# Kernel optimization log

Measured on AMD Instinct MI355X. Metric: run time of the kernel, lower is better.

Reference implementation:

```python
import jax, jax.numpy as jnp
from jax import lax
import numpy as np

B, T, F, U = 256, 150, 1024, 28


def setup_inputs() -> dict:
    key = jax.random.key(0)
    ks = jax.random.split(key, 10)
    s = 0.05  # keep tanh/sigmoid unsaturated, ~glorot magnitude
    return {
        "x": jax.random.normal(ks[0], (B, T, F), jnp.float32),
        "Wa": jax.random.normal(ks[1], (U, F), jnp.float32) * s,
        "Ua": jax.random.normal(ks[2], (F, F), jnp.float32) * s,
        "Va": jax.random.normal(ks[3], (F, 1), jnp.float32) * s,
        "Ba1": jax.random.normal(ks[4], (1, F), jnp.float32) * s,
        "Ba2": jax.random.normal(ks[5], (1, F), jnp.float32) * s,
        "Ba3": jax.random.normal(ks[6], (1, 1), jnp.float32) * s,
        "gru_kernel": jax.random.normal(ks[7], (F, 3 * U), jnp.float32) * s,
        "gru_rkernel": jax.random.normal(ks[8], (U, 3 * U), jnp.float32) * s,
        "gru_bias": jax.random.normal(ks[9], (2, 3 * U), jnp.float32) * s,
    }


def reference(x, Wa, Ua, Va, Ba1, Ba2, Ba3, gru_kernel, gru_rkernel, gru_bias):
    b, t, f = x.shape
    u = Wa.shape[0]
    # UaH is loop-invariant in the original (x @ Ua + Ba2 each step) -> hoist it.
    UaH = jnp.einsum('btf,fg->btg', x, Ua) + Ba2  # (B,T,F)

    def step(h, _):
        # Bahdanau attention conditioned on previous GRU state h (B,U)
        WaS = h @ Wa + Ba1                                    # (B,F)
        scores = jnp.einsum('btf,fo->bt', jnp.tanh(UaH + WaS[:, None, :]), Va) + Ba3[0, 0]
        a = jax.nn.softmax(scores, axis=1)                    # (B,T)
        ctx = jnp.einsum('btf,bt->bf', x, a)                  # (B,F)
        # Keras GRUCell (reset_after=True)
        xz = ctx @ gru_kernel + gru_bias[0]                   # (B,3U)
        hz = h @ gru_rkernel + gru_bias[1]                    # (B,3U)
        x_z, x_r, x_h = jnp.split(xz, 3, axis=-1)
        r_z, r_r, r_h = jnp.split(hz, 3, axis=-1)
        z = jax.nn.sigmoid(x_z + r_z)
        r = jax.nn.sigmoid(x_r + r_r)
        hh = jnp.tanh(x_h + r * r_h)
        h_new = z * h + (1.0 - z) * hh
        return h_new, h_new

    h0 = jnp.zeros((b, u), x.dtype)
    _, ys = lax.scan(step, h0, None, length=t)  # (T,B,U)
    return jnp.transpose(ys, (1, 0, 2))         # (B,T,U)
```

## Files before the change

### kernel.cpp

```cpp
#include <hip/hip_runtime.h>
#include <hip/hip_bf16.h>


typedef _Float16 h8 __attribute__((ext_vector_type(8)));
typedef _Float16 h4 __attribute__((ext_vector_type(4)));
typedef _Float16 h2 __attribute__((ext_vector_type(2)));
typedef float    f4 __attribute__((ext_vector_type(4)));
typedef float    f2 __attribute__((ext_vector_type(2)));

#define B_   256
#define T_   150
#define F_   1024
#define U_   28
#define TU3  84

#define C2LOG2E 2.8853900817779268f
#define LOG2E   1.4426950408889634f

__device__ __forceinline__ float fast_exp(float x) {
    return __builtin_amdgcn_exp2f(x * LOG2E);
}
__device__ __forceinline__ float fast_sigmoid(float x) {
    float e = __builtin_amdgcn_exp2f(-x * LOG2E);
    return __builtin_amdgcn_rcpf(1.0f + e);
}
__device__ __forceinline__ float fast_tanh(float x) {
    float e = __builtin_amdgcn_exp2f(x * C2LOG2E);
    float r = __builtin_amdgcn_rcpf(e + 1.0f);
    return 1.0f - 2.0f * r;
}

__global__ void k_cvt(const float* __restrict__ in, _Float16* __restrict__ out, int n4) {
    int i = blockIdx.x * blockDim.x + threadIdx.x;
    int stride = gridDim.x * blockDim.x;
    const f4* in4 = (const f4*)in;
    h4* out4 = (h4*)out;
    for (; i < n4; i += stride) {
        f4 v = in4[i];
        h4 o;
        o[0] = (_Float16)v[0]; o[1] = (_Float16)v[1];
        o[2] = (_Float16)v[2]; o[3] = (_Float16)v[3];
        out4[i] = o;
    }
}

__global__ void k_cvt_transpose(const float* __restrict__ in, _Float16* __restrict__ out) {
    int idx = blockIdx.x * blockDim.x + threadIdx.x;
    int r = idx >> 10, c = idx & 1023;
    out[(c << 10) + r] = (_Float16)in[idx];
}

#define BM 128
#define BN 128
#define BK 32
#define LDT 40

__global__ __launch_bounds__(256) void k_gemm(
    const _Float16* __restrict__ A,
    const _Float16* __restrict__ Bt,
    const float*    __restrict__ bias,
    _Float16*       __restrict__ C)
{
    __shared__ _Float16 As[BM][LDT];
    __shared__ _Float16 Bs[BN][LDT];
    const int K = 1024;
    int bm = blockIdx.y, bn = blockIdx.x;
    int tid = threadIdx.x;
    int lane = tid & 63, wid = tid >> 6;
    int wm = wid >> 1, wn = wid & 1;
    f4 acc[4][4];
#pragma unroll
    for (int i = 0; i < 4; i++)
#pragma unroll
        for (int j = 0; j < 4; j++) { f4 z = {0.f, 0.f, 0.f, 0.f}; acc[i][j] = z; }

    int row0 = bm * BM, col0 = bn * BN;
    for (int kt = 0; kt < K; kt += BK) {
#pragma unroll
        for (int p = 0; p < 2; ++p) {
            int s = tid + p * 256;
            int r = s >> 2, seg = s & 3;
            h8 va = *(const h8*)(A  + (size_t)(row0 + r) * K + kt + seg * 8);
            *(h8*)(&As[r][seg * 8]) = va;
            h8 vb = *(const h8*)(Bt + (size_t)(col0 + r) * K + kt + seg * 8);
            *(h8*)(&Bs[r][seg * 8]) = vb;
        }
        __syncthreads();
        int kq = (lane >> 4) * 8;
        h8 af[4], bf[4];
#pragma unroll
        for (int mi = 0; mi < 4; mi++) af[mi] = *(const h8*)(&As[wm * 64 + mi * 16 + (lane & 15)][kq]);
#pragma unroll
        for (int ni = 0; ni < 4; ni++) bf[ni] = *(const h8*)(&Bs[wn * 64 + ni * 16 + (lane & 15)][kq]);
#pragma unroll
        for (int mi = 0; mi < 4; mi++)
#pragma unroll
            for (int ni = 0; ni < 4; ni++)
                acc[mi][ni] = __builtin_amdgcn_mfma_f32_16x16x32_f16(af[mi], bf[ni], acc[mi][ni], 0, 0, 0);
        __syncthreads();
    }
    int rq = (lane >> 4) * 4, cq = lane & 15;
#pragma unroll
    for (int mi = 0; mi < 4; mi++)
#pragma unroll
        for (int ni = 0; ni < 4; ni++) {
            int gc = col0 + wn * 64 + ni * 16 + cq;
            float bv = bias[gc];
#pragma unroll
            for (int j = 0; j < 4; j++) {
                int gr = row0 + wm * 64 + mi * 16 + rq + j;
                C[(size_t)gr * 1024 + gc] = (_Float16)(acc[mi][ni][j] + bv);
            }
        }
}

#define XLD 72

__global__ __launch_bounds__(256) void k_gemm_xg(
    const _Float16* __restrict__ A,
    const float*    __restrict__ gk,
    _Float16*       __restrict__ C)
{
    __shared__ _Float16 As[128][XLD];
    __shared__ _Float16 Bs[96][XLD];
    int tid = threadIdx.x;
    int lane = tid & 63, wid = tid >> 6;
    int wm = wid >> 1, wn = wid & 1;
    int row0 = blockIdx.x * 128;
    f4 acc[4][3];
#pragma unroll
    for (int i = 0; i < 4; i++)
#pragma unroll
        for (int j = 0; j < 3; j++) { f4 z = {0.f, 0.f, 0.f, 0.f}; acc[i][j] = z; }

    if (tid < 432) { h2 z; z[0] = (_Float16)0.f; z[1] = (_Float16)0.f; ((h2*)&Bs[84][0])[tid] = z; }

    for (int kt = 0; kt < 1024; kt += 64) {
#pragma unroll
        for (int p = 0; p < 4; ++p) {
            int s = tid + p * 256;
            int r = s >> 3, seg = s & 7;
            *(h8*)(&As[r][seg * 8]) = *(const h8*)(A + (size_t)(row0 + r) * 1024 + kt + seg * 8);
        }
#pragma unroll
        for (int p = 0; p < 21; ++p) {
            int s = tid + p * 256;
            int j = s % 84, k = s / 84;
            Bs[j][k] = (_Float16)gk[(size_t)(kt + k) * 84 + j];
        }
        __syncthreads();
#pragma unroll
        for (int kk = 0; kk < 64; kk += 32) {
            int kq = kk + (lane >> 4) * 8;
            h8 af[4], bf[3];
#pragma unroll
            for (int mi = 0; mi < 4; mi++) af[mi] = *(const h8*)(&As[wm * 64 + mi * 16 + (lane & 15)][kq]);
#pragma unroll
            for (int ni = 0; ni < 3; ni++) bf[ni] = *(const h8*)(&Bs[wn * 48 + ni * 16 + (lane & 15)][kq]);
#pragma unroll
            for (int mi = 0; mi < 4; mi++)
#pragma unroll
                for (int ni = 0; ni < 3; ni++)
                    acc[mi][ni] = __builtin_amdgcn_mfma_f32_16x16x32_f16(af[mi], bf[ni], acc[mi][ni], 0, 0, 0);
        }
        __syncthreads();
    }
    int rq = (lane >> 4) * 4, cq = lane & 15;
#pragma unroll
    for (int mi = 0; mi < 4; mi++)
#pragma unroll
        for (int ni = 0; ni < 3; ni++) {
            int gc = wn * 48 + ni * 16 + cq;
            if (gc < 84) {
#pragma unroll
                for (int j = 0; j < 4; j++) {
                    int gr = row0 + wm * 64 + mi * 16 + rq + j;
                    C[(size_t)gr * 84 + gc] = (_Float16)acc[mi][ni][j];
                }
            }
        }
}

__global__ __launch_bounds__(1024) void k_recur2(
    const _Float16* __restrict__ uah,
    const _Float16* __restrict__ xg,
    const float* __restrict__ Wa,
    const float* __restrict__ Va,
    const float* __restrict__ Ba1,
    const float* __restrict__ grk,
    const float* __restrict__ gbias,
    float* __restrict__ out)
{
    __shared__ _Float16 sWa[U_ * F_];
    __shared__ _Float16 sXG[T_ * TU3];
    __shared__ float sWaS[F_];
    __shared__ float sScore[160];
    __shared__ float sPart[8 * TU3];
    __shared__ float sGrk[U_ * TU3];
    __shared__ float sHz[TU3];
    __shared__ float sH[U_];
    __shared__ float sDen;

    int b = blockIdx.x;
    int tid = threadIdx.x;
    int lane = tid & 63, wvid = tid >> 6;

    for (int i = tid; i < U_ * F_; i += 1024) sWa[i] = (_Float16)Wa[i];
    {
        const _Float16* xgb = xg + (size_t)b * T_ * TU3;
        for (int i = tid; i < T_ * TU3; i += 1024) sXG[i] = xgb[i];
    }
    for (int i = tid; i < U_ * TU3; i += 1024) sGrk[i] = grk[i];
    if (tid < U_) sH[tid] = 0.f;

    float rBa1 = Ba1[tid];
    float rA0[8], rA1[8], vaBase = 0.f;
    {
        f4 a0 = *(const f4*)(Va + 8 * lane);
        f4 a1 = *(const f4*)(Va + 8 * lane + 4);
        f4 b0 = *(const f4*)(Va + 512 + 8 * lane);
        f4 b1 = *(const f4*)(Va + 512 + 8 * lane + 4);
#pragma unroll
        for (int e = 0; e < 4; ++e) {
            rA0[e] = -2.f * a0[e]; rA0[4 + e] = -2.f * a1[e];
            rA1[e] = -2.f * b0[e]; rA1[4 + e] = -2.f * b1[e];
            vaBase += a0[e] + a1[e] + b0[e] + b1[e];
        }
    }
    int p4c = tid / TU3, p4j = tid - p4c * TU3;
    bool p4on = tid < 8 * TU3;
    bool denon = (wvid == 13);
    bool hzon = (tid >= 896) && (tid < 896 + TU3);
    int hj = tid - 896;
    float rGb1 = hzon ? gbias[TU3 + hj] : 0.f;
    float rG0 = 0.f, rG1 = 0.f, rG2 = 0.f;
    if (tid < U_) { rG0 = gbias[tid]; rG1 = gbias[U_ + tid]; rG2 = gbias[2 * U_ + tid]; }
    __syncthreads();

    const _Float16* ub = uah + (size_t)b * T_ * F_;
    float* ob = out + (size_t)b * T_ * U_;

    for (int t = 0; t < T_; ++t) {
        {
            float acc = rBa1;
#pragma unroll
            for (int u = 0; u < U_; ++u) acc += sH[u] * (float)sWa[u * F_ + tid];
            sWaS[tid] = acc;
        }
        __syncthreads();
        float rW0[8], rW1[8];
        {
            f4 a0 = *(const f4*)(sWaS + 8 * lane);
            f4 a1 = *(const f4*)(sWaS + 8 * lane + 4);
            f4 b0 = *(const f4*)(sWaS + 512 + 8 * lane);
            f4 b1 = *(const f4*)(sWaS + 512 + 8 * lane + 4);
#pragma unroll
            for (int e = 0; e < 4; ++e) {
                rW0[e] = a0[e] * C2LOG2E; rW0[4 + e] = a1[e] * C2LOG2E;
                rW1[e] = b0[e] * C2LOG2E; rW1[4 + e] = b1[e] * C2LOG2E;
            }
        }
        {
            int r = wvid;
            const h8* pr = (const h8*)(ub + (size_t)r * F_);
            h8 u0 = pr[lane], u1 = pr[64 + lane];
            while (r < T_) {
                int rn = r + 16;
                h8 n0, n1;
                if (rn < T_) {
                    const h8* pn = (const h8*)(ub + (size_t)rn * F_);
                    n0 = pn[lane]; n1 = pn[64 + lane];
                }
                float acc = vaBase;
#pragma unroll
                for (int e = 0; e < 8; ++e) {
                    float t0 = fmaf((float)u0[e], C2LOG2E, rW0[e]);
                    float r0 = __builtin_amdgcn_rcpf(__builtin_amdgcn_exp2f(t0) + 1.0f);
                    acc = fmaf(rA0[e], r0, acc);
                    float t1 = fmaf((float)u1[e], C2LOG2E, rW1[e]);
                    float r1 = __builtin_amdgcn_rcpf(__builtin_amdgcn_exp2f(t1) + 1.0f);
                    acc = fmaf(rA1[e], r1, acc);
                }
#pragma unroll
                for (int off = 32; off; off >>= 1) acc += __shfl_xor(acc, off, 64);
                if (lane == 0) sScore[r] = fast_exp(acc);
                u0 = n0; u1 = n1; r = rn;
            }
        }
        __syncthreads();
        if (p4on) {
            float acc = 0.f;
            for (int r = p4c; r < T_; r += 8)
                acc = fmaf((float)sXG[r * TU3 + p4j], sScore[r], acc);
            sPart[p4c * TU3 + p4j] = acc;
        }
        if (denon) {
            float d0 = (lane < T_)       ? sScore[lane]       : 0.f;
            float d1 = (lane + 64 < T_)  ? sScore[lane + 64]  : 0.f;
            float d2 = (lane + 128 < T_) ? sScore[lane + 128] : 0.f;
            float ds = d0 + d1 + d2;
#pragma unroll
            for (int off = 32; off; off >>= 1) ds += __shfl_xor(ds, off, 64);
            if (lane == 0) sDen = ds;
        }
        if (hzon) {
            float hz = rGb1;
#pragma unroll
            for (int u = 0; u < U_; ++u) hz += sH[u] * sGrk[u * TU3 + hj];
            sHz[hj] = hz;
        }
        __syncthreads();
        if (tid < U_) {
            float rs = __builtin_amdgcn_rcpf(sDen);
            float x0 = 0.f, x1 = 0.f, x2 = 0.f;
#pragma unroll
            for (int c = 0; c < 8; ++c) {
                x0 += sPart[c * TU3 + tid];
                x1 += sPart[c * TU3 + U_ + tid];
                x2 += sPart[c * TU3 + 2 * U_ + tid];
            }
            x0 = fmaf(x0, rs, rG0);
            x1 = fmaf(x1, rs, rG1);
            x2 = fmaf(x2, rs, rG2);
            float z  = fast_sigmoid(x0 + sHz[tid]);
            float r  = fast_sigmoid(x1 + sHz[U_ + tid]);
            float hh = fast_tanh(x2 + r * sHz[2 * U_ + tid]);
            float hn = z * sH[tid] + (1.f - z) * hh;
            sH[tid] = hn;
            ob[(size_t)t * U_ + tid] = hn;
        }
        __syncthreads();
    }
}

extern "C" void kernel_launch(void* const* d_in, const int* in_sizes, int n_in,
                              void* d_out, int out_size, void* d_ws, size_t ws_size,
                              hipStream_t stream) {
    (void)in_sizes; (void)n_in; (void)out_size; (void)ws_size;
    const float* x   = (const float*)d_in[0];
    const float* Wa  = (const float*)d_in[1];
    const float* Ua  = (const float*)d_in[2];
    const float* Va  = (const float*)d_in[3];
    const float* Ba1 = (const float*)d_in[4];
    const float* Ba2 = (const float*)d_in[5];
    const float* gk  = (const float*)d_in[7];
    const float* grk = (const float*)d_in[8];
    const float* gb  = (const float*)d_in[9];
    float* out = (float*)d_out;

    const size_t NX = (size_t)B_ * T_ * F_;
    _Float16* xh  = (_Float16*)d_ws;
    _Float16* uat = xh + NX;
    _Float16* uah = uat + (size_t)F_ * F_;
    _Float16* xgh = uah + NX;

    k_cvt<<<2048, 256, 0, stream>>>(x, xh, (int)(NX / 4));
    k_cvt_transpose<<<(F_ * F_) / 256, 256, 0, stream>>>(Ua, uat);
    dim3 gg(F_ / BN, (B_ * T_) / BM);
    k_gemm<<<gg, 256, 0, stream>>>(xh, uat, Ba2, uah);
    k_gemm_xg<<<(B_ * T_) / 128, 256, 0, stream>>>(xh, gk, xgh);
    k_recur2<<<B_, 1024, 0, stream>>>(uah, xgh, Wa, Va, Ba1, grk, gb, out);
}
```

Baseline: 2.231 ms.

## Precompute exp of UaH in GEMM epilogue and factor tanh exponent in recurrence

The Ua GEMM epilogue now stores exp(2*(UaH)) in fp16, clamped to stay in range. The recurrence then forms tanh terms as 1/(1+E*D), where D=exp(2*WaS) is computed once per step, which removes one exp per element from the inner loop of all 150 steps. Wa and the hidden state move into registers as packed half pairs, the context partial sums are split into 16 groups over half2 data, and the row loop processes two rows per iteration. The clamp and fp16 storage of the exponential values lower precision and can change results when pre-activations are large.

```diff
diff --git a/kernel.cpp b/kernel.cpp
--- a/kernel.cpp
+++ b/kernel.cpp
@@ -109,7 +109,8 @@
 #pragma unroll
             for (int j = 0; j < 4; j++) {
                 int gr = row0 + wm * 64 + mi * 16 + rq + j;
-                C[(size_t)gr * 1024 + gc] = (_Float16)(acc[mi][ni][j] + bv);
+                float ex = __builtin_amdgcn_exp2f(fminf(C2LOG2E * (acc[mi][ni][j] + bv), 15.8f));
+                C[(size_t)gr * 1024 + gc] = (_Float16)ex;
             }
         }
 }
@@ -181,8 +182,8 @@
         }
 }
 
-__global__ __launch_bounds__(1024) void k_recur2(
-    const _Float16* __restrict__ uah,
+__global__ __launch_bounds__(1024) void k_recur3(
+    const _Float16* __restrict__ Eg,
     const _Float16* __restrict__ xg,
     const float* __restrict__ Wa,
     const float* __restrict__ Va,
@@ -191,28 +192,36 @@
     const float* __restrict__ gbias,
     float* __restrict__ out)
 {
-    __shared__ _Float16 sWa[U_ * F_];
-    __shared__ _Float16 sXG[T_ * TU3];
+    __shared__ h2    sXG2[T_ * 42];
     __shared__ float sWaS[F_];
     __shared__ float sScore[160];
-    __shared__ float sPart[8 * TU3];
-    __shared__ float sGrk[U_ * TU3];
+    __shared__ f2    sPart2[16 * 42];
+    __shared__ h2    sGrkT[TU3 * 14];
     __shared__ float sHz[TU3];
-    __shared__ float sH[U_];
+    __shared__ h2    sH2[14];
     __shared__ float sDen;
 
     int b = blockIdx.x;
     int tid = threadIdx.x;
     int lane = tid & 63, wvid = tid >> 6;
 
-    for (int i = tid; i < U_ * F_; i += 1024) sWa[i] = (_Float16)Wa[i];
     {
-        const _Float16* xgb = xg + (size_t)b * T_ * TU3;
-        for (int i = tid; i < T_ * TU3; i += 1024) sXG[i] = xgb[i];
-    }
-    for (int i = tid; i < U_ * TU3; i += 1024) sGrk[i] = grk[i];
-    if (tid < U_) sH[tid] = 0.f;
-
+        const h2* xgb = (const h2*)(xg + (size_t)b * T_ * TU3);
+        for (int i = tid; i < T_ * 42; i += 1024) sXG2[i] = xgb[i];
+    }
+    for (int i = tid; i < TU3 * 14; i += 1024) {
+        int j = i / 14, k = i - j * 14;
+        h2 g; g[0] = (_Float16)grk[(2 * k) * TU3 + j]; g[1] = (_Float16)grk[(2 * k + 1) * TU3 + j];
+        sGrkT[i] = g;
+    }
+    if (tid < 14) { h2 z; z[0] = (_Float16)0.f; z[1] = (_Float16)0.f; sH2[tid] = z; }
+
+    h2 wreg[14];
+#pragma unroll
+    for (int k = 0; k < 14; ++k) {
+        h2 w; w[0] = (_Float16)Wa[(2 * k) * F_ + tid]; w[1] = (_Float16)Wa[(2 * k + 1) * F_ + tid];
+        wreg[k] = w;
+    }
     float rBa1 = Ba1[tid];
     float rA0[8], rA1[8], vaBase = 0.f;
     {
@@ -227,28 +236,35 @@
             vaBase += a0[e] + a1[e] + b0[e] + b1[e];
         }
     }
-    int p4c = tid / TU3, p4j = tid - p4c * TU3;
-    bool p4on = tid < 8 * TU3;
+    int p4g = tid / 42, p4j = tid - p4g * 42;
+    bool p4on = tid < 16 * 42;
     bool denon = (wvid == 13);
     bool hzon = (tid >= 896) && (tid < 896 + TU3);
     int hj = tid - 896;
     float rGb1 = hzon ? gbias[TU3 + hj] : 0.f;
     float rG0 = 0.f, rG1 = 0.f, rG2 = 0.f;
     if (tid < U_) { rG0 = gbias[tid]; rG1 = gbias[U_ + tid]; rG2 = gbias[2 * U_ + tid]; }
+    float hPrev = 0.f;
     __syncthreads();
 
-    const _Float16* ub = uah + (size_t)b * T_ * F_;
+    const _Float16* ub = Eg + (size_t)b * T_ * F_;
     float* ob = out + (size_t)b * T_ * U_;
 
     for (int t = 0; t < T_; ++t) {
+        h2 hh[14];
+#pragma unroll
+        for (int k = 0; k < 14; ++k) hh[k] = sH2[k];
         {
             float acc = rBa1;
 #pragma unroll
-            for (int u = 0; u < U_; ++u) acc += sH[u] * (float)sWa[u * F_ + tid];
+            for (int k = 0; k < 14; ++k) {
+                acc = fmaf((float)hh[k][0], (float)wreg[k][0], acc);
+                acc = fmaf((float)hh[k][1], (float)wreg[k][1], acc);
+            }
             sWaS[tid] = acc;
         }
         __syncthreads();
-        float rW0[8], rW1[8];
+        float rD0[8], rD1[8];
         {
             f4 a0 = *(const f4*)(sWaS + 8 * lane);
             f4 a1 = *(const f4*)(sWaS + 8 * lane + 4);
@@ -256,43 +272,68 @@
             f4 b1 = *(const f4*)(sWaS + 512 + 8 * lane + 4);
 #pragma unroll
             for (int e = 0; e < 4; ++e) {
-                rW0[e] = a0[e] * C2LOG2E; rW0[4 + e] = a1[e] * C2LOG2E;
-                rW1[e] = b0[e] * C2LOG2E; rW1[4 + e] = b1[e] * C2LOG2E;
+                rD0[e]     = __builtin_amdgcn_exp2f(C2LOG2E * a0[e]);
+                rD0[4 + e] = __builtin_amdgcn_exp2f(C2LOG2E * a1[e]);
+                rD1[e]     = __builtin_amdgcn_exp2f(C2LOG2E * b0[e]);
+                rD1[4 + e] = __builtin_amdgcn_exp2f(C2LOG2E * b1[e]);
             }
         }
         {
             int r = wvid;
-            const h8* pr = (const h8*)(ub + (size_t)r * F_);
-            h8 u0 = pr[lane], u1 = pr[64 + lane];
-            while (r < T_) {
-                int rn = r + 16;
-                h8 n0, n1;
-                if (rn < T_) {
-                    const h8* pn = (const h8*)(ub + (size_t)rn * F_);
-                    n0 = pn[lane]; n1 = pn[64 + lane];
+            for (; r + 16 < T_; r += 32) {
+                const h8* p1 = (const h8*)(ub + (size_t)r * F_);
+                const h8* p2 = (const h8*)(ub + (size_t)(r + 16) * F_);
+                h8 a0 = p1[lane], a1 = p1[64 + lane];
+                h8 b0 = p2[lane], b1 = p2[64 + lane];
+                float s1 = vaBase, s2 = vaBase;
+#pragma unroll
+                for (int e = 0; e < 8; ++e) {
+                    float m0 = fmaf((float)a0[e], rD0[e], 0.f);
+                    s1 = fmaf(rA0[e], __builtin_amdgcn_rcpf(1.0f + m0), s1);
+                    float m1 = fmaf((float)a1[e], rD1[e], 0.f);
+                    s1 = fmaf(rA1[e], __builtin_amdgcn_rcpf(1.0f + m1), s1);
+                    float n0 = fmaf((float)b0[e], rD0[e], 0.f);
+                    s2 = fmaf(rA0[e], __builtin_amdgcn_rcpf(1.0f + n0), s2);
+                    float n1 = fmaf((float)b1[e], rD1[e], 0.f);
+                    s2 = fmaf(rA1[e], __builtin_amdgcn_rcpf(1.0f + n1), s2);
                 }
-                float acc = vaBase;
+#pragma unroll
+                for (int off = 32; off; off >>= 1) {
+                    s1 += __shfl_xor(s1, off, 64);
+                    s2 += __shfl_xor(s2, off, 64);
+                }
+                if (lane == 0) {
+                    sScore[r]      = fast_exp(s1);
+                    sScore[r + 16] = fast_exp(s2);
+                }
+            }
+            if (r < T_) {
+                const h8* p1 = (const h8*)(ub + (size_t)r * F_);
+                h8 a0 = p1[lane], a1 = p1[64 + lane];
+                float s1 = vaBase;
 #pragma unroll
                 for (int e = 0; e < 8; ++e) {
-                    float t0 = fmaf((float)u0[e], C2LOG2E, rW0[e]);
-                    float r0 = __builtin_amdgcn_rcpf(__builtin_amdgcn_exp2f(t0) + 1.0f);
-                    acc = fmaf(rA0[e], r0, acc);
-                    float t1 = fmaf((float)u1[e], C2LOG2E, rW1[e]);
-                    float r1 = __builtin_amdgcn_rcpf(__builtin_amdgcn_exp2f(t1) + 1.0f);
-                    acc = fmaf(rA1[e], r1, acc);
+                    float m0 = fmaf((float)a0[e], rD0[e], 0.f);
+                    s1 = fmaf(rA0[e], __builtin_amdgcn_rcpf(1.0f + m0), s1);
+                    float m1 = fmaf((float)a1[e], rD1[e], 0.f);
+                    s1 = fmaf(rA1[e], __builtin_amdgcn_rcpf(1.0f + m1), s1);
                 }
 #pragma unroll
-                for (int off = 32; off; off >>= 1) acc += __shfl_xor(acc, off, 64);
-                if (lane == 0) sScore[r] = fast_exp(acc);
-                u0 = n0; u1 = n1; r = rn;
+                for (int off = 32; off; off >>= 1) s1 += __shfl_xor(s1, off, 64);
+                if (lane == 0) sScore[r] = fast_exp(s1);
             }
         }
         __syncthreads();
         if (p4on) {
-            float acc = 0.f;
-            for (int r = p4c; r < T_; r += 8)
-                acc = fmaf((float)sXG[r * TU3 + p4j], sScore[r], acc);
-            sPart[p4c * TU3 + p4j] = acc;
+            float acc0 = 0.f, acc1 = 0.f;
+            for (int r = p4g; r < T_; r += 16) {
+                h2 m2 = sXG2[r * 42 + p4j];
+                float s = sScore[r];
+                acc0 = fmaf((float)m2[0], s, acc0);
+                acc1 = fmaf((float)m2[1], s, acc1);
+            }
+            f2 pv; pv[0] = acc0; pv[1] = acc1;
+            sPart2[p4g * 42 + p4j] = pv;
         }
         if (denon) {
             float d0 = (lane < T_)       ? sScore[lane]       : 0.f;
@@ -306,28 +347,41 @@
         if (hzon) {
             float hz = rGb1;
 #pragma unroll
-            for (int u = 0; u < U_; ++u) hz += sH[u] * sGrk[u * TU3 + hj];
+            for (int k = 0; k < 14; ++k) {
+                h2 g = sGrkT[hj * 14 + k];
+                hz = fmaf((float)hh[k][0], (float)g[0], hz);
+                hz = fmaf((float)hh[k][1], (float)g[1], hz);
+            }
             sHz[hj] = hz;
         }
         __syncthreads();
+        float hn = 0.f;
         if (tid < U_) {
+            const float* sp = (const float*)sPart2;
             float rs = __builtin_amdgcn_rcpf(sDen);
             float x0 = 0.f, x1 = 0.f, x2 = 0.f;
 #pragma unroll
-            for (int c = 0; c < 8; ++c) {
-                x0 += sPart[c * TU3 + tid];
-                x1 += sPart[c * TU3 + U_ + tid];
-                x2 += sPart[c * TU3 + 2 * U_ + tid];
+            for (int c = 0; c < 16; ++c) {
+                x0 += sp[c * 84 + tid];
+                x1 += sp[c * 84 + U_ + tid];
+                x2 += sp[c * 84 + 2 * U_ + tid];
             }
             x0 = fmaf(x0, rs, rG0);
             x1 = fmaf(x1, rs, rG1);
             x2 = fmaf(x2, rs, rG2);
             float z  = fast_sigmoid(x0 + sHz[tid]);
             float r  = fast_sigmoid(x1 + sHz[U_ + tid]);
-            float hh = fast_tanh(x2 + r * sHz[2 * U_ + tid]);
-            float hn = z * sH[tid] + (1.f - z) * hh;
-            sH[tid] = hn;
+            float hhat = fast_tanh(x2 + r * sHz[2 * U_ + tid]);
+            hn = z * hPrev + (1.f - z) * hhat;
+            hPrev = hn;
             ob[(size_t)t * U_ + tid] = hn;
+        }
+        if (wvid == 0) {
+            float other = __shfl_xor(hn, 1, 64);
+            if (tid < U_ && !(tid & 1)) {
+                h2 hv; hv[0] = (_Float16)hn; hv[1] = (_Float16)other;
+                sH2[tid >> 1] = hv;
+            }
         }
         __syncthreads();
     }
@@ -351,13 +405,13 @@
     const size_t NX = (size_t)B_ * T_ * F_;
     _Float16* xh  = (_Float16*)d_ws;
     _Float16* uat = xh + NX;
-    _Float16* uah = uat + (size_t)F_ * F_;
-    _Float16* xgh = uah + NX;
+    _Float16* eg  = uat + (size_t)F_ * F_;
+    _Float16* xgh = eg + NX;
 
     k_cvt<<<2048, 256, 0, stream>>>(x, xh, (int)(NX / 4));
     k_cvt_transpose<<<(F_ * F_) / 256, 256, 0, stream>>>(Ua, uat);
     dim3 gg(F_ / BN, (B_ * T_) / BM);
-    k_gemm<<<gg, 256, 0, stream>>>(xh, uat, Ba2, uah);
+    k_gemm<<<gg, 256, 0, stream>>>(xh, uat, Ba2, eg);
     k_gemm_xg<<<(B_ * T_) / 128, 256, 0, stream>>>(xh, gk, xgh);
-    k_recur2<<<B_, 1024, 0, stream>>>(uah, xgh, Wa, Va, Ba1, grk, gb, out);
-}
+    k_recur3<<<B_, 1024, 0, stream>>>(eg, xgh, Wa, Va, Ba1, grk, gb, out);
+}
```

After: 2.291 ms. 1.03x slower.
